# Performance work log

Hardware: AMD Instinct MI355X
Metric: run time of the kernel (lower is better)

## Reference

```python
import jax, jax.numpy as jnp
import numpy as np

KERNEL_SIZE = 128
SEQ_LEN = 4096
BATCH = 8192
OUT_LEN = SEQ_LEN - KERNEL_SIZE + 1
LR = 1.0


def setup_inputs() -> dict:
    key = jax.random.key(0)
    k1, k2, k3, k4 = jax.random.split(key, 4)
    x = jax.random.normal(k1, (1, BATCH, SEQ_LEN), dtype=jnp.float32)
    # BCE-style labels in [0, 1]
    y = (jax.random.uniform(k2, (1, BATCH, 1)) > 0.5).astype(jnp.float32)
    kernel = jax.random.normal(k3, (1, KERNEL_SIZE, 1), dtype=jnp.float32) * 0.1
    bias = jax.random.normal(k4, (1, 1, 1), dtype=jnp.float32) * 0.1
    return {"x": x, "y": y, "kernel": kernel, "bias": bias}


def reference(x, y, kernel, bias):
    # x: (1, B, L); kernel: (1, K, 1); bias: (1, 1, 1); y: (1, B, 1)
    K = kernel.shape[1]
    out_len = x.shape[-1] - K + 1
    batch = x.shape[1]

    # --- forward: sum_i (x[:, :, i:i+K] @ kernel) + out_len * bias ---
    # sum over windows collapses to one weighted sum along L:
    #   pooled[b] = sum_j x[b, j] * c[j],  c[j] = sum_k kernel[k] * 1[0 <= j-k < out_len]
    # i.e. c = full convolution of kernel with a window of ones (length L).
    c = jnp.convolve(kernel[0, :, 0], jnp.ones((out_len,), x.dtype), mode="full")  # (L,)
    pooled_sum = jnp.einsum("obl,l->ob", x, c)[..., None] + out_len * bias  # (1, B, 1)

    logits = pooled_sum / out_len
    output = jax.nn.sigmoid(logits)

    # --- manual backward (as in the module) ---
    d_logits = output - y
    d_conv = d_logits / out_len  # (1, B, 1)

    # d_kernel[k] = (1/batch) * sum_b d_conv[b] * S[b, k],
    # S[b, k] = sum_{i=0}^{out_len-1} x[b, i+k]  (sliding-window sum via cumsum)
    cs = jnp.cumsum(jnp.pad(x, ((0, 0), (0, 0), (1, 0))), axis=-1)  # (1, B, L+1)
    S = cs[:, :, out_len:out_len + K] - cs[:, :, :K]  # (1, B, K)
    d_kernel = jnp.einsum("obk,obj->okj", S, d_conv) / batch  # (1, K, 1)

    # d_bias accumulates the same batch-sum out_len times
    d_bias = out_len * jnp.sum(d_conv, axis=1, keepdims=True) / batch  # (1, 1, 1)

    kernel_new = kernel - LR * d_kernel
    bias_new = bias - LR * d_bias
    return (kernel_new, bias_new)
```

## Files before the change

kernel.cpp:

```cpp
#include <hip/hip_runtime.h>
#include <math.h>

#define SEQ_LEN 4096
#define KSZ 128
#define OUT_LEN 3969
#define BATCH 8192
#define NB_MAIN 256
#define NWAVES 16
#define TAIL_NB 16

template <int CTRL>
__device__ __forceinline__ float dpp_add(float x) {
    const int m = __builtin_amdgcn_update_dpp(0, __float_as_int(x), CTRL, 0xf, 0xf, true);
    return x + __int_as_float(m);
}
__device__ __forceinline__ float wave_sum_uniform(float x) {
    x = dpp_add<0x111>(x);
    x = dpp_add<0x112>(x);
    x = dpp_add<0x114>(x);
    x = dpp_add<0x118>(x);
    x = dpp_add<0x142>(x);
    x = dpp_add<0x143>(x);
    return __int_as_float(__builtin_amdgcn_readlane(__float_as_int(x), 63));
}

__global__ __launch_bounds__(1024)
__attribute__((amdgpu_waves_per_eu(4, 4)))
void conv1d_train_main(
    const float* __restrict__ x, const float* __restrict__ y,
    const float* __restrict__ kern, const float* __restrict__ bias,
    float* __restrict__ partial)
{
    __shared__ float P[KSZ];
    __shared__ float sl[NWAVES][256];

    const int tid  = threadIdx.x;
    const int wave = tid >> 6;
    const int lane = tid & 63;

    if (tid < KSZ) P[tid] = kern[tid];
    __syncthreads();
#pragma unroll
    for (int off = 1; off < KSZ; off <<= 1) {
        float v = 0.f;
        if (tid < KSZ) {
            v = P[tid];
            if (tid >= off) v += P[tid - off];
        }
        __syncthreads();
        if (tid < KSZ) P[tid] = v;
        __syncthreads();
    }
    const float ksum = P[KSZ - 1];
    const float bs   = bias[0];

    float w0, w1, w2, w3;
    if (lane < 32) {
        const int j = 4 * lane;
        w0 = P[j] - ksum; w1 = P[j + 1] - ksum;
        w2 = P[j + 2] - ksum; w3 = P[j + 3] - ksum;
    } else {
        const int m = 4 * (lane - 32) - 1;
        w0 = (m >= 0) ? -P[m] : 0.f;
        w1 = -P[m + 1]; w2 = -P[m + 2]; w3 = -P[m + 3];
    }

    float g0 = 0.f, g1 = 0.f, g2 = 0.f, g3 = 0.f;
    float C0 = 0.f, db = 0.f;

    const int wg = blockIdx.x * NWAVES + wave;

    for (int b = wg; b < BATCH; b += NB_MAIN * NWAVES) {
        const float4* xr = reinterpret_cast<const float4*>(x + (size_t)b * SEQ_LEN);
        float4 r[16];
#pragma unroll
        for (int i = 0; i < 16; ++i) r[i] = xr[i * 64 + lane];
        const float yv = y[b];

        float tot = 0.f;
#pragma unroll
        for (int i = 0; i < 16; ++i) tot += (r[i].x + r[i].y) + (r[i].z + r[i].w);

        const float4 e = (lane < 32) ? r[0] : r[15];
        const float corr = ((w0 * e.x + w1 * e.y) + (w2 * e.z + w3 * e.w));

        const float t = wave_sum_uniform(tot);
        const float c = wave_sum_uniform(corr);

        const float logits = (ksum * t + c) * (1.f / (float)OUT_LEN) + bs;
        const float sig    = 1.f / (1.f + expf(-logits));
        const float dconv  = (sig - yv) * (1.f / (float)OUT_LEN);

        g0 += dconv * e.x; g1 += dconv * e.y;
        g2 += dconv * e.z; g3 += dconv * e.w;
        C0 += dconv * t;   db += dconv;
    }

    if (lane < 32) {
        const int j = 4 * lane;
        sl[wave][j]     = g0;
        sl[wave][j + 1] = g1;
        sl[wave][j + 2] = g2;
        if (j + 3 < 127) sl[wave][j + 3] = g3;
    } else {
        const int s0 = 4 * lane - 1;
        if (lane > 32) sl[wave][s0] = g0;
        sl[wave][s0 + 1] = g1;
        sl[wave][s0 + 2] = g2;
        sl[wave][s0 + 3] = g3;
    }
    if (lane == 0) { sl[wave][127] = C0; sl[wave][255] = db; }
    __syncthreads();
    if (tid < 256) {
        float s = 0.f;
#pragma unroll
        for (int w = 0; w < NWAVES; ++w) s += sl[w][tid];
        partial[(size_t)blockIdx.x * 256 + tid] = s;
    }
}

__global__ __launch_bounds__(1024) void conv1d_train_tail(
    const float* __restrict__ partial, float* __restrict__ accum,
    unsigned* __restrict__ counter,
    const float* __restrict__ kern, const float* __restrict__ bias,
    float* __restrict__ out)
{
    __shared__ float slr[NWAVES][256];
    __shared__ float colsum[256];
    __shared__ float sc[256];
    __shared__ unsigned lastFlag;

    const int tid   = threadIdx.x;
    const int rsub  = tid >> 6;
    const int f4c   = tid & 63;
    const int rbase = blockIdx.x * 16;

    const float4* p4 = reinterpret_cast<const float4*>(partial);
    const float4 v = p4[(size_t)(rbase + rsub) * 64 + f4c];
    slr[rsub][4 * f4c + 0] = v.x;
    slr[rsub][4 * f4c + 1] = v.y;
    slr[rsub][4 * f4c + 2] = v.z;
    slr[rsub][4 * f4c + 3] = v.w;
    __syncthreads();

    if (tid < 256) {
        float s = 0.f;
#pragma unroll
        for (int w = 0; w < NWAVES; ++w) s += slr[w][tid];
        atomicExch(&accum[(size_t)blockIdx.x * 256 + tid], s);
    }
    __syncthreads();

    if (tid == 0) {
        __threadfence();
        const unsigned old = atomicAdd(counter, 1u);
        lastFlag = ((old & 15u) == 15u) ? 1u : 0u;
    }
    __syncthreads();
    if (!lastFlag) return;

    {
        const int w4 = tid >> 8;
        const int c  = tid & 255;
        float s = 0.f;
#pragma unroll
        for (int w = 0; w < 4; ++w)
            s += __hip_atomic_load(&accum[(size_t)(w4 + 4 * w) * 256 + c],
                                   __ATOMIC_RELAXED, __HIP_MEMORY_SCOPE_AGENT);
        slr[w4][c] = s;
    }
    __syncthreads();
    if (tid < 256)
        colsum[tid] = (slr[0][tid] + slr[1][tid]) + (slr[2][tid] + slr[3][tid]);
    __syncthreads();

    float gh = 0.f;
    if (tid < 256) {
        gh = colsum[tid];
        if (tid == 127 || tid == 255) gh = 0.f;
        sc[tid] = gh;
    }
    __syncthreads();
#pragma unroll
    for (int off = 1; off < 128; off <<= 1) {
        float add = 0.f;
        if (tid < 256 && (tid & 127) >= off) add = sc[tid - off];
        __syncthreads();
        if (tid < 256) sc[tid] += add;
        __syncthreads();
    }

    if (tid < 128) {
        const float C0   = colsum[127];
        const float TH   = sc[255];
        const float pre  = sc[tid] - gh;
        const float inch = sc[128 + tid];
        const float h_t  = (tid < 127) ? colsum[128 + tid] : 0.f;
        const float suf  = TH - (inch - h_t);
        const float dk = (C0 - pre - suf) * (1.f / (float)BATCH);
        out[tid] = kern[tid] - dk;
    }
    if (tid == 0) {
        const float dbo = colsum[255] * ((float)OUT_LEN / (float)BATCH);
        out[128] = bias[0] - dbo;
    }
}

extern "C" void kernel_launch(void* const* d_in, const int* in_sizes, int n_in,
                              void* d_out, int out_size, void* d_ws, size_t ws_size,
                              hipStream_t stream) {
    (void)in_sizes; (void)n_in; (void)out_size; (void)ws_size;
    const float* x    = (const float*)d_in[0];
    const float* y    = (const float*)d_in[1];
    const float* kern = (const float*)d_in[2];
    const float* bias = (const float*)d_in[3];
    float* out = (float*)d_out;

    float*    partial = (float*)d_ws;
    float*    accum   = partial + (size_t)NB_MAIN * 256;
    unsigned* counter = (unsigned*)(accum + (size_t)TAIL_NB * 256);

    hipLaunchKernelGGL(conv1d_train_main, dim3(NB_MAIN), dim3(1024), 0, stream,
                       x, y, kern, bias, partial);
    hipLaunchKernelGGL(conv1d_train_tail, dim3(TAIL_NB), dim3(1024), 0, stream,
                       partial, accum, counter, kern, bias, out);
}
```

Before: 31.26 us.

## Fuse main and tail kernels into one launch with atomic-counter two-level reduction

Merges the per-block partial reduction and the tail reduction into one kernel. The last 16 blocks to arrive at a global counter spin until all 256 blocks have published, then each reduces 16 rows into a second level, and a second counter picks the final block to produce the kernel and bias update. This removes a second kernel launch and its boundary gap, but adds a hipMemsetAsync to reset the counters and a spin-wait whose safety assumes all 256 blocks are co-resident.

```diff
diff --git a/kernel.cpp b/kernel.cpp
--- a/kernel.cpp
+++ b/kernel.cpp
@@ -7,7 +7,6 @@
 #define BATCH 8192
 #define NB_MAIN 256
 #define NWAVES 16
-#define TAIL_NB 16
 
 template <int CTRL>
 __device__ __forceinline__ float dpp_add(float x) {
@@ -24,15 +23,24 @@
     return __int_as_float(__builtin_amdgcn_readlane(__float_as_int(x), 63));
 }
 
+__device__ __forceinline__ float agent_load(const float* p) {
+    return __hip_atomic_load(p, __ATOMIC_RELAXED, __HIP_MEMORY_SCOPE_AGENT);
+}
+
 __global__ __launch_bounds__(1024)
 __attribute__((amdgpu_waves_per_eu(4, 4)))
-void conv1d_train_main(
+void conv1d_train_fused(
     const float* __restrict__ x, const float* __restrict__ y,
     const float* __restrict__ kern, const float* __restrict__ bias,
-    float* __restrict__ partial)
+    float* __restrict__ lvl1, float* __restrict__ lvl2,
+    unsigned* __restrict__ cnt1, unsigned* __restrict__ cnt2,
+    float* __restrict__ out)
 {
     __shared__ float P[KSZ];
     __shared__ float sl[NWAVES][256];
+    __shared__ float colsum[256];
+    __shared__ float sc[256];
+    __shared__ unsigned shRank;
 
     const int tid  = threadIdx.x;
     const int wave = tid >> 6;
@@ -111,67 +119,67 @@
     }
     if (lane == 0) { sl[wave][127] = C0; sl[wave][255] = db; }
     __syncthreads();
+
     if (tid < 256) {
         float s = 0.f;
 #pragma unroll
         for (int w = 0; w < NWAVES; ++w) s += sl[w][tid];
-        partial[(size_t)blockIdx.x * 256 + tid] = s;
-    }
-}
-
-__global__ __launch_bounds__(1024) void conv1d_train_tail(
-    const float* __restrict__ partial, float* __restrict__ accum,
-    unsigned* __restrict__ counter,
-    const float* __restrict__ kern, const float* __restrict__ bias,
-    float* __restrict__ out)
-{
-    __shared__ float slr[NWAVES][256];
-    __shared__ float colsum[256];
-    __shared__ float sc[256];
-    __shared__ unsigned lastFlag;
-
-    const int tid   = threadIdx.x;
-    const int rsub  = tid >> 6;
-    const int f4c   = tid & 63;
-    const int rbase = blockIdx.x * 16;
-
-    const float4* p4 = reinterpret_cast<const float4*>(partial);
-    const float4 v = p4[(size_t)(rbase + rsub) * 64 + f4c];
-    slr[rsub][4 * f4c + 0] = v.x;
-    slr[rsub][4 * f4c + 1] = v.y;
-    slr[rsub][4 * f4c + 2] = v.z;
-    slr[rsub][4 * f4c + 3] = v.w;
-    __syncthreads();
-
+        atomicExch(&lvl1[(size_t)blockIdx.x * 256 + tid], s);
+    }
+    __syncthreads();
+
+    if (tid == 0) {
+        const unsigned rank = __hip_atomic_fetch_add(
+            cnt1, 1u, __ATOMIC_ACQ_REL, __HIP_MEMORY_SCOPE_AGENT);
+        shRank = rank;
+        if (rank >= (unsigned)(NB_MAIN - 16)) {
+            while (__hip_atomic_load(cnt1, __ATOMIC_ACQUIRE,
+                                     __HIP_MEMORY_SCOPE_AGENT)
+                   < (unsigned)NB_MAIN) {}
+        }
+    }
+    __syncthreads();
+    const unsigned rank1 = shRank;
+    if (rank1 < (unsigned)(NB_MAIN - 16)) return;
+
+    const int c = (int)(rank1 - (unsigned)(NB_MAIN - 16));
+    {
+        const int rsub = tid >> 6;
+        const int f4c  = tid & 63;
+        const float* rowp = lvl1 + (size_t)(16 * c + rsub) * 256 + 4 * f4c;
+        sl[rsub][4 * f4c + 0] = agent_load(rowp + 0);
+        sl[rsub][4 * f4c + 1] = agent_load(rowp + 1);
+        sl[rsub][4 * f4c + 2] = agent_load(rowp + 2);
+        sl[rsub][4 * f4c + 3] = agent_load(rowp + 3);
+    }
+    __syncthreads();
     if (tid < 256) {
         float s = 0.f;
 #pragma unroll
-        for (int w = 0; w < NWAVES; ++w) s += slr[w][tid];
-        atomicExch(&accum[(size_t)blockIdx.x * 256 + tid], s);
-    }
-    __syncthreads();
-
+        for (int w = 0; w < NWAVES; ++w) s += sl[w][tid];
+        atomicExch(&lvl2[(size_t)c * 256 + tid], s);
+    }
+    __syncthreads();
     if (tid == 0) {
-        __threadfence();
-        const unsigned old = atomicAdd(counter, 1u);
-        lastFlag = ((old & 15u) == 15u) ? 1u : 0u;
-    }
-    __syncthreads();
-    if (!lastFlag) return;
+        const unsigned old2 = __hip_atomic_fetch_add(
+            cnt2, 1u, __ATOMIC_ACQ_REL, __HIP_MEMORY_SCOPE_AGENT);
+        shRank = old2;
+    }
+    __syncthreads();
+    if (shRank != 15u) return;
 
     {
         const int w4 = tid >> 8;
-        const int c  = tid & 255;
+        const int cc = tid & 255;
         float s = 0.f;
 #pragma unroll
         for (int w = 0; w < 4; ++w)
-            s += __hip_atomic_load(&accum[(size_t)(w4 + 4 * w) * 256 + c],
-                                   __ATOMIC_RELAXED, __HIP_MEMORY_SCOPE_AGENT);
-        slr[w4][c] = s;
+            s += agent_load(&lvl2[(size_t)(w4 + 4 * w) * 256 + cc]);
+        sl[w4][cc] = s;
     }
     __syncthreads();
     if (tid < 256)
-        colsum[tid] = (slr[0][tid] + slr[1][tid]) + (slr[2][tid] + slr[3][tid]);
+        colsum[tid] = (sl[0][tid] + sl[1][tid]) + (sl[2][tid] + sl[3][tid]);
     __syncthreads();
 
     float gh = 0.f;
@@ -191,13 +199,13 @@
     }
 
     if (tid < 128) {
-        const float C0   = colsum[127];
+        const float C0a  = colsum[127];
         const float TH   = sc[255];
         const float pre  = sc[tid] - gh;
         const float inch = sc[128 + tid];
         const float h_t  = (tid < 127) ? colsum[128 + tid] : 0.f;
         const float suf  = TH - (inch - h_t);
-        const float dk = (C0 - pre - suf) * (1.f / (float)BATCH);
+        const float dk = (C0a - pre - suf) * (1.f / (float)BATCH);
         out[tid] = kern[tid] - dk;
     }
     if (tid == 0) {
@@ -216,12 +224,12 @@
     const float* bias = (const float*)d_in[3];
     float* out = (float*)d_out;
 
-    float*    partial = (float*)d_ws;
-    float*    accum   = partial + (size_t)NB_MAIN * 256;
-    unsigned* counter = (unsigned*)(accum + (size_t)TAIL_NB * 256);
-
-    hipLaunchKernelGGL(conv1d_train_main, dim3(NB_MAIN), dim3(1024), 0, stream,
-                       x, y, kern, bias, partial);
-    hipLaunchKernelGGL(conv1d_train_tail, dim3(TAIL_NB), dim3(1024), 0, stream,
-                       partial, accum, counter, kern, bias, out);
-}
+    float*    lvl1 = (float*)d_ws;
+    float*    lvl2 = lvl1 + (size_t)NB_MAIN * 256;
+    unsigned* cnt1 = (unsigned*)(lvl2 + (size_t)16 * 256);
+    unsigned* cnt2 = cnt1 + 1;
+
+    hipMemsetAsync(cnt1, 0, 2 * sizeof(unsigned), stream);
+    hipLaunchKernelGGL(conv1d_train_fused, dim3(NB_MAIN), dim3(1024), 0, stream,
+                       x, y, kern, bias, lvl1, lvl2, cnt1, cnt2, out);
+}
```

New measurement: 41.53 us. 1.33x slower.
